# Kernel optimization log

Hardware: AMD Instinct MI355X
Metric: run time of the kernel (lower is better)

Reference implementation:

```python
import jax, jax.numpy as jnp
import numpy as np

N = 50000   # nodes
E = 800000  # edges
G = 256     # graphs in batch
H = 64      # hidden_dim
L = 4       # residual blocks
EPS = 1e-5


def setup_inputs() -> dict:
    key = jax.random.key(0)
    ks = jax.random.split(key, 12)
    s = 0.05
    return dict(
        x=jax.random.normal(ks[0], (N, 3), dtype=jnp.float32),
        edge_index=jax.random.randint(ks[1], (2, E), 0, N, dtype=jnp.int32),
        batch=jnp.sort(jax.random.randint(ks[2], (N,), 0, G, dtype=jnp.int32)),
        proj_W=jax.random.normal(ks[3], (3, H)) * s,
        proj_b=jnp.zeros((H,)),
        conv_W=jax.random.normal(ks[4], (L, 2, H, H)) * s,   # [block, conv1/2, in, out]
        conv_b=jnp.zeros((L, 2, H)),
        bn_g=jnp.ones((L, 2, H)),
        bn_b=jnp.zeros((L, 2, H)),
        lin1_W=jax.random.normal(ks[5], (2 * H, H)) * s,
        lin1_b=jnp.zeros((H,)),
        lin2_W=jax.random.normal(ks[6], (H, H // 2)) * s,
        lin2_b=jnp.zeros((H // 2,)),
        lin3_W=jax.random.normal(ks[7], (H // 2, 2)) * s,
        lin3_b=jnp.zeros((2,)),
        bnf1_g=jnp.ones((H,)), bnf1_b=jnp.zeros((H,)),
        bnf2_g=jnp.ones((H // 2,)), bnf2_b=jnp.zeros((H // 2,)),
    )


def _bn(x, g, b):
    # training-mode BatchNorm1d over the node axis (biased variance)
    m = x.mean(axis=0)
    v = x.var(axis=0)
    return (x - m) * jax.lax.rsqrt(v + EPS) * g + b


def _gcn(h, W, b, src, dst, dis):
    # GCNConv with self-loops and symmetric normalization:
    # out_i = sum_{j->i} d_j^-1/2 d_i^-1/2 (h_j W) + d_i^-1 (h_i W) + b
    hw = h @ W
    msg = hw[src] * (dis[src] * dis[dst])[:, None]          # [E, H] gather
    agg = jax.ops.segment_sum(msg, dst, num_segments=h.shape[0])
    agg = agg + hw * (dis * dis)[:, None]                    # self loops
    return agg + b


def reference(x, edge_index, batch, proj_W, proj_b, conv_W, conv_b, bn_g, bn_b,
              lin1_W, lin1_b, lin2_W, lin2_b, lin3_W, lin3_b,
              bnf1_g, bnf1_b, bnf2_g, bnf2_b):
    src, dst = edge_index[0], edge_index[1]
    n = x.shape[0]
    # degree on A + I (self-loops), computed on destination index
    deg = jax.ops.segment_sum(jnp.ones((src.shape[0],), x.dtype), dst, num_segments=n) + 1.0
    dis = jax.lax.rsqrt(deg)

    h = x @ proj_W + proj_b
    for l in range(L):
        idn = h
        o = _gcn(h, conv_W[l, 0], conv_b[l, 0], src, dst, dis)
        o = jax.nn.relu(_bn(o, bn_g[l, 0], bn_b[l, 0]))
        o = _gcn(o, conv_W[l, 1], conv_b[l, 1], src, dst, dis)
        o = _bn(o, bn_g[l, 1], bn_b[l, 1])
        h = jax.nn.relu(o + idn)

    cnt = jax.ops.segment_sum(jnp.ones((n,), h.dtype), batch, num_segments=G)
    x_mean = jax.ops.segment_sum(h, batch, num_segments=G) / jnp.maximum(cnt, 1.0)[:, None]
    x_max = jax.ops.segment_max(h, batch, num_segments=G)
    x_max = jnp.where(jnp.isfinite(x_max), x_max, 0.0)  # guard empty graphs

    z = jnp.concatenate([x_mean, x_max], axis=1)
    z = jax.nn.relu(_bn(z @ lin1_W + lin1_b, bnf1_g, bnf1_b))
    z = jax.nn.relu(_bn(z @ lin2_W + lin2_b, bnf2_g, bnf2_b))
    return z @ lin3_W + lin3_b
```

## Files before the change

kernel.cpp:

```cpp
#include <hip/hip_runtime.h>
#include <hip/hip_bf16.h>
#include <cstdint>
#include <cstddef>

#define N_NODES 50000
#define N_EDGES 800000
#define G_GRAPHS 256
#define H_DIM 64
#define EPS_BN 1e-5f

__global__ void k_deg(const int* __restrict__ dst, int* __restrict__ cnt) {
    int e = blockIdx.x * 256 + threadIdx.x;
    if (e < N_EDGES) atomicAdd(&cnt[dst[e]], 1);
}

__global__ __launch_bounds__(1024) void k_scan_dis(const int* __restrict__ cnt,
                                                   int* __restrict__ row_ptr,
                                                   float* __restrict__ dis) {
    __shared__ int sh[1024];
    int t = threadIdx.x;
    int base = t * 49;
    int s = 0;
    for (int j = 0; j < 49; j++) {
        int i = base + j;
        if (i < N_NODES) {
            int c = cnt[i];
            dis[i] = rsqrtf((float)c + 1.0f);
            s += c;
        }
    }
    sh[t] = s;
    __syncthreads();
    for (int off = 1; off < 1024; off <<= 1) {
        int v = sh[t];
        int v2 = (t >= off) ? sh[t - off] : 0;
        __syncthreads();
        sh[t] = v + v2;
        __syncthreads();
    }
    int run = sh[t] - s;
    for (int j = 0; j < 49; j++) {
        int i = base + j;
        if (i < N_NODES) { row_ptr[i] = run; run += cnt[i]; }
        else if (i == N_NODES) { row_ptr[i] = run; }
    }
}

__global__ void k_scatter(const int* __restrict__ src, const int* __restrict__ dst,
                          const int* __restrict__ row_ptr, int* __restrict__ cursor,
                          int* __restrict__ csr) {
    int e = blockIdx.x * 256 + threadIdx.x;
    if (e < N_EDGES) {
        int d = dst[e];
        int p = atomicAdd(&cursor[d], 1);
        csr[row_ptr[d] + p] = src[e];
    }
}

__global__ void k_proj(const float* __restrict__ x, const float* __restrict__ W,
                       const float* __restrict__ b, float* __restrict__ h) {
    int tid = blockIdx.x * 256 + threadIdx.x;
    int i = tid >> 6, c = tid & 63;
    if (i < N_NODES) {
        float x0 = x[i * 3], x1 = x[i * 3 + 1], x2 = x[i * 3 + 2];
        h[tid] = x0 * W[c] + x1 * W[64 + c] + x2 * W[128 + c] + b[c];
    }
}

template <int MODE>
__global__ __launch_bounds__(256) void k_gemm(const float* __restrict__ in,
                                              const float* __restrict__ Wg,
                                              const float* __restrict__ dis,
                                              const float* __restrict__ coef,
                                              float* __restrict__ out) {
    __shared__ float Wt[64 * 64];
    __shared__ float hT[64 * 65];
    __shared__ float sA[64], sSh[64];
    int t = threadIdx.x;
    int nb = blockIdx.x * 64;

    if (MODE == 1 && t < 64) { sA[t] = coef[t]; sSh[t] = coef[64 + t]; }
    __syncthreads();

    const float4* W4 = (const float4*)Wg;
    float4* Wt4 = (float4*)Wt;
#pragma unroll
    for (int i = 0; i < 4; i++) Wt4[t + 256 * i] = W4[t + 256 * i];

    int srow = t >> 4, c4 = t & 15;
#pragma unroll
    for (int i = 0; i < 4; i++) {
        int r = srow + 16 * i;
        int node = nb + r;
        float4 v = make_float4(0.f, 0.f, 0.f, 0.f);
        if (node < N_NODES) v = *(const float4*)&in[(size_t)node * 64 + c4 * 4];
        float e0 = v.x, e1 = v.y, e2 = v.z, e3 = v.w;
        if (MODE == 1) {
            int c = c4 * 4;
            e0 = fmaxf(e0 * sA[c] + sSh[c], 0.f);
            e1 = fmaxf(e1 * sA[c + 1] + sSh[c + 1], 0.f);
            e2 = fmaxf(e2 * sA[c + 2] + sSh[c + 2], 0.f);
            e3 = fmaxf(e3 * sA[c + 3] + sSh[c + 3], 0.f);
        }
        float* dr = &hT[r * 65 + c4 * 4];
        dr[0] = e0; dr[1] = e1; dr[2] = e2; dr[3] = e3;
    }
    __syncthreads();

    int c0 = (t & 15) * 4, n0 = (t >> 4) * 4;
    float acc[4][4];
#pragma unroll
    for (int j = 0; j < 4; j++)
#pragma unroll
        for (int i = 0; i < 4; i++) acc[j][i] = 0.f;

#pragma unroll 16
    for (int k = 0; k < 64; k++) {
        float4 wv = *(float4*)&Wt[k * 64 + c0];
        float h0 = hT[(n0 + 0) * 65 + k];
        float h1 = hT[(n0 + 1) * 65 + k];
        float h2 = hT[(n0 + 2) * 65 + k];
        float h3 = hT[(n0 + 3) * 65 + k];
        acc[0][0] += h0 * wv.x; acc[0][1] += h0 * wv.y; acc[0][2] += h0 * wv.z; acc[0][3] += h0 * wv.w;
        acc[1][0] += h1 * wv.x; acc[1][1] += h1 * wv.y; acc[1][2] += h1 * wv.z; acc[1][3] += h1 * wv.w;
        acc[2][0] += h2 * wv.x; acc[2][1] += h2 * wv.y; acc[2][2] += h2 * wv.z; acc[2][3] += h2 * wv.w;
        acc[3][0] += h3 * wv.x; acc[3][1] += h3 * wv.y; acc[3][2] += h3 * wv.z; acc[3][3] += h3 * wv.w;
    }

#pragma unroll
    for (int j = 0; j < 4; j++) {
        int node = nb + n0 + j;
        if (node < N_NODES) {
            float d = dis[node];
            float4 o;
            o.x = acc[j][0] * d; o.y = acc[j][1] * d; o.z = acc[j][2] * d; o.w = acc[j][3] * d;
            *(float4*)&out[(size_t)node * 64 + c0] = o;
        }
    }
}

__global__ __launch_bounds__(256) void k_agg(const float* __restrict__ hwn,
                                             const int* __restrict__ row_ptr,
                                             const int* __restrict__ csr,
                                             const float* __restrict__ dis,
                                             float* __restrict__ o,
                                             float* __restrict__ partial) {
    int t = threadIdx.x;
    int w = t >> 6, lane = t & 63;
    int gw = blockIdx.x * 4 + w;
    float sS = 0.f, sQ = 0.f;
    for (int i = gw; i < N_NODES; i += 4096) {
        float v = hwn[(size_t)i * 64 + lane];
        int beg = row_ptr[i], end = row_ptr[i + 1];
        int e = beg;
        for (; e + 4 <= end; e += 4) {
            int s0 = csr[e], s1 = csr[e + 1], s2 = csr[e + 2], s3 = csr[e + 3];
            float v0 = hwn[(size_t)s0 * 64 + lane];
            float v1 = hwn[(size_t)s1 * 64 + lane];
            float v2 = hwn[(size_t)s2 * 64 + lane];
            float v3 = hwn[(size_t)s3 * 64 + lane];
            v += (v0 + v1) + (v2 + v3);
        }
        for (; e < end; e++) v += hwn[(size_t)csr[e] * 64 + lane];
        v *= dis[i];
        o[(size_t)i * 64 + lane] = v;
        sS += v; sQ += v * v;
    }
    __shared__ float red[4][128];
    red[w][lane] = sS;
    red[w][64 + lane] = sQ;
    __syncthreads();
    if (t < 128) {
        float p = red[0][t] + red[1][t] + red[2][t] + red[3][t];
        partial[blockIdx.x * 128 + t] = p;
    }
}

__global__ __launch_bounds__(512) void k_fin(const float* __restrict__ partial,
                                             const float* __restrict__ g,
                                             const float* __restrict__ b,
                                             float* __restrict__ coef) {
    __shared__ float sh[4][128];
    __shared__ float st[128];
    int t = threadIdx.x;
    int c = t & 127, q = t >> 7;
    float acc = 0.f;
#pragma unroll 4
    for (int r = q; r < 1024; r += 4) acc += partial[r * 128 + c];
    sh[q][c] = acc;
    __syncthreads();
    if (t < 128) st[t] = sh[0][t] + sh[1][t] + sh[2][t] + sh[3][t];
    __syncthreads();
    if (t < 64) {
        float S = st[t], Q = st[t + 64];
        float mean = S * (1.0f / N_NODES);
        float var = Q * (1.0f / N_NODES) - mean * mean;
        float a = g[t] * rsqrtf(var + EPS_BN);
        coef[t] = a;
        coef[64 + t] = b[t] - mean * a;
    }
}

__global__ void k_res(const float* __restrict__ o2, const float* __restrict__ hold,
                      const float* __restrict__ coef, float* __restrict__ hnew) {
    int t4 = blockIdx.x * 256 + threadIdx.x;
    size_t base = (size_t)t4 * 4;
    int c0 = (int)(base & 63);
    float4 o = *(const float4*)&o2[base];
    float4 hi = *(const float4*)&hold[base];
    float4 r;
    r.x = fmaxf(o.x * coef[c0 + 0] + coef[64 + c0 + 0] + hi.x, 0.f);
    r.y = fmaxf(o.y * coef[c0 + 1] + coef[64 + c0 + 1] + hi.y, 0.f);
    r.z = fmaxf(o.z * coef[c0 + 2] + coef[64 + c0 + 2] + hi.z, 0.f);
    r.w = fmaxf(o.w * coef[c0 + 3] + coef[64 + c0 + 3] + hi.w, 0.f);
    *(float4*)&hnew[base] = r;
}

__global__ void k_gbound(const int* __restrict__ batch, int* __restrict__ gstart) {
    int g = threadIdx.x;
    int lo = 0, hi = N_NODES;
    while (lo < hi) {
        int mid = (lo + hi) >> 1;
        if (batch[mid] < g) lo = mid + 1; else hi = mid;
    }
    gstart[g] = lo;
    if (g == 0) gstart[G_GRAPHS] = N_NODES;
}

__global__ __launch_bounds__(256) void k_pool(const float* __restrict__ h,
                                              const int* __restrict__ gstart,
                                              float* __restrict__ pmean,
                                              float* __restrict__ pmax) {
    int g = blockIdx.x;
    int s = gstart[g], e = gstart[g + 1];
    int t = threadIdx.x, w = t >> 6, lane = t & 63;
    float sum = 0.f, mx = 0.f;
    for (int i = s + w; i < e; i += 4) {
        float v = h[(size_t)i * 64 + lane];
        sum += v;
        mx = fmaxf(mx, v);
    }
    __shared__ float rs[4][64], rm[4][64];
    rs[w][lane] = sum;
    rm[w][lane] = mx;
    __syncthreads();
    if (t < 64) {
        float S = rs[0][t] + rs[1][t] + rs[2][t] + rs[3][t];
        float M = fmaxf(fmaxf(rm[0][t], rm[1][t]), fmaxf(rm[2][t], rm[3][t]));
        float cntf = (float)(e - s);
        pmean[g * 64 + t] = S / fmaxf(cntf, 1.0f);
        pmax[g * 64 + t] = M;
    }
}

__global__ __launch_bounds__(512) void k_head(const float* __restrict__ pmean,
                                              const float* __restrict__ pmax,
                                              const float* __restrict__ W1,
                                              const float* __restrict__ W2,
                                              const float* __restrict__ W3,
                                              const float* __restrict__ b3,
                                              const float* __restrict__ g1, const float* __restrict__ bb1,
                                              const float* __restrict__ g2, const float* __restrict__ bb2,
                                              float* __restrict__ ybuf, float* __restrict__ y2buf,
                                              float* __restrict__ outp) {
    int t = threadIdx.x;
    int w = t >> 6, lane = t & 63;
    int rgrp = w & 3, chalf = w >> 2;
    int r = rgrp * 64 + lane;
    __shared__ float pstat[8][32][2];
    __shared__ float aC[64], shC[64];

    float acc[32];
#pragma unroll
    for (int c = 0; c < 32; c++) acc[c] = 0.f;
    int c0 = chalf * 32;
    for (int kc = 0; kc < 4; kc++) {
        float zk[32];
#pragma unroll
        for (int j = 0; j < 32; j++) {
            int k = kc * 32 + j;
            zk[j] = (k < 64) ? pmean[r * 64 + k] : pmax[r * 64 + (k - 64)];
        }
        for (int j = 0; j < 32; j++) {
            float z = zk[j];
            int k = kc * 32 + j;
#pragma unroll
            for (int cq = 0; cq < 8; cq++) {
                float4 wv = *(const float4*)&W1[k * 64 + c0 + cq * 4];
                acc[cq * 4 + 0] += z * wv.x;
                acc[cq * 4 + 1] += z * wv.y;
                acc[cq * 4 + 2] += z * wv.z;
                acc[cq * 4 + 3] += z * wv.w;
            }
        }
    }
    for (int c = 0; c < 32; c++) {
        float v = acc[c], q = acc[c] * acc[c];
        for (int m = 1; m < 64; m <<= 1) { v += __shfl_xor(v, m, 64); q += __shfl_xor(q, m, 64); }
        if (lane == 0) { pstat[w][c][0] = v; pstat[w][c][1] = q; }
    }
    __syncthreads();
    if (t < 64) {
        int ch = t >> 5, cc = t & 31;
        float S = 0.f, Q = 0.f;
        for (int i = 0; i < 4; i++) { S += pstat[ch * 4 + i][cc][0]; Q += pstat[ch * 4 + i][cc][1]; }
        float mean = S * (1.f / 256.f), var = Q * (1.f / 256.f) - mean * mean;
        float a = g1[t] * rsqrtf(var + EPS_BN);
        aC[t] = a;
        shC[t] = bb1[t] - mean * a;
    }
    __syncthreads();
    for (int c = 0; c < 32; c++) {
        float y = fmaxf(acc[c] * aC[c0 + c] + shC[c0 + c], 0.f);
        ybuf[r * 64 + c0 + c] = y;
    }
    __syncthreads();

    float acc2[16];
#pragma unroll
    for (int c = 0; c < 16; c++) acc2[c] = 0.f;
    int c0b = chalf * 16;
    for (int kc = 0; kc < 2; kc++) {
        float yk[32];
#pragma unroll
        for (int j = 0; j < 32; j++) yk[j] = ybuf[r * 64 + kc * 32 + j];
        for (int j = 0; j < 32; j++) {
            float y = yk[j];
            int k = kc * 32 + j;
#pragma unroll
            for (int cq = 0; cq < 4; cq++) {
                float4 wv = *(const float4*)&W2[k * 32 + c0b + cq * 4];
                acc2[cq * 4 + 0] += y * wv.x;
                acc2[cq * 4 + 1] += y * wv.y;
                acc2[cq * 4 + 2] += y * wv.z;
                acc2[cq * 4 + 3] += y * wv.w;
            }
        }
    }
    for (int c = 0; c < 16; c++) {
        float v = acc2[c], q = acc2[c] * acc2[c];
        for (int m = 1; m < 64; m <<= 1) { v += __shfl_xor(v, m, 64); q += __shfl_xor(q, m, 64); }
        if (lane == 0) { pstat[w][c][0] = v; pstat[w][c][1] = q; }
    }
    __syncthreads();
    if (t < 32) {
        int ch = t >> 4, cc = t & 15;
        float S = 0.f, Q = 0.f;
        for (int i = 0; i < 4; i++) { S += pstat[ch * 4 + i][cc][0]; Q += pstat[ch * 4 + i][cc][1]; }
        float mean = S * (1.f / 256.f), var = Q * (1.f / 256.f) - mean * mean;
        float a = g2[t] * rsqrtf(var + EPS_BN);
        aC[t] = a;
        shC[t] = bb2[t] - mean * a;
    }
    __syncthreads();
    for (int c = 0; c < 16; c++) {
        float y = fmaxf(acc2[c] * aC[c0b + c] + shC[c0b + c], 0.f);
        y2buf[r * 32 + c0b + c] = y;
    }
    __syncthreads();

    if (chalf == 0) {
        float o0 = b3[0], o1 = b3[1];
        for (int j = 0; j < 32; j++) {
            float y = y2buf[r * 32 + j];
            o0 += y * W3[j * 2];
            o1 += y * W3[j * 2 + 1];
        }
        outp[r * 2] = o0;
        outp[r * 2 + 1] = o1;
    }
}

extern "C" void kernel_launch(void* const* d_in, const int* in_sizes, int n_in,
                              void* d_out, int out_size, void* d_ws, size_t ws_size,
                              hipStream_t stream) {
    (void)in_sizes; (void)n_in; (void)out_size; (void)ws_size;
    const float* x      = (const float*)d_in[0];
    const int*   ei     = (const int*)d_in[1];
    const int*   batch  = (const int*)d_in[2];
    const float* proj_W = (const float*)d_in[3];
    const float* proj_b = (const float*)d_in[4];
    const float* conv_W = (const float*)d_in[5];
    const float* bn_g   = (const float*)d_in[7];
    const float* bn_b   = (const float*)d_in[8];
    const float* lin1_W = (const float*)d_in[9];
    const float* lin2_W = (const float*)d_in[11];
    const float* lin3_W = (const float*)d_in[13];
    const float* lin3_b = (const float*)d_in[14];
    const float* bnf1_g = (const float*)d_in[15];
    const float* bnf1_b = (const float*)d_in[16];
    const float* bnf2_g = (const float*)d_in[17];
    const float* bnf2_b = (const float*)d_in[18];
    const int* srcp = ei;
    const int* dstp = ei + N_EDGES;

    char* ws = (char*)d_ws;
    auto alloc = [&](size_t bytes) {
        char* p = ws;
        ws += (bytes + 255) / 256 * 256;
        return p;
    };
    int*   cnt     = (int*)alloc((size_t)N_NODES * 4);
    float* dis     = (float*)alloc((size_t)N_NODES * 4);
    int*   row_ptr = (int*)alloc((size_t)(N_NODES + 1) * 4);
    int*   cursor  = (int*)alloc((size_t)N_NODES * 4);
    int*   csr     = (int*)alloc((size_t)N_EDGES * 4);
    float* BA      = (float*)alloc((size_t)N_NODES * 64 * 4);
    float* BB      = (float*)alloc((size_t)N_NODES * 64 * 4);
    float* BC      = (float*)alloc((size_t)N_NODES * 64 * 4);
    float* partial = (float*)alloc((size_t)1024 * 128 * 4);
    float* coef    = (float*)alloc(128 * 4);
    float* pmean   = (float*)alloc((size_t)G_GRAPHS * 64 * 4);
    float* pmax    = (float*)alloc((size_t)G_GRAPHS * 64 * 4);
    int*   gstart  = (int*)alloc((size_t)(G_GRAPHS + 1) * 4);
    float* ybuf    = (float*)alloc((size_t)G_GRAPHS * 64 * 4);
    float* y2buf   = (float*)alloc((size_t)G_GRAPHS * 32 * 4);

    hipMemsetAsync(cnt, 0, (size_t)N_NODES * 4, stream);
    hipMemsetAsync(cursor, 0, (size_t)N_NODES * 4, stream);

    k_deg<<<3125, 256, 0, stream>>>(dstp, cnt);
    k_scan_dis<<<1, 1024, 0, stream>>>(cnt, row_ptr, dis);
    k_scatter<<<3125, 256, 0, stream>>>(srcp, dstp, row_ptr, cursor, csr);
    k_proj<<<12500, 256, 0, stream>>>(x, proj_W, proj_b, BA);

    float* A = BA; float* B = BB; float* C = BC;
    for (int l = 0; l < 4; l++) {
        const float* W0 = conv_W + (size_t)(l * 2 + 0) * 4096;
        const float* W1c = conv_W + (size_t)(l * 2 + 1) * 4096;
        k_gemm<0><<<782, 256, 0, stream>>>(A, W0, dis, nullptr, B);
        k_agg<<<1024, 256, 0, stream>>>(B, row_ptr, csr, dis, C, partial);
        k_fin<<<1, 512, 0, stream>>>(partial, bn_g + (l * 2) * 64, bn_b + (l * 2) * 64, coef);
        k_gemm<1><<<782, 256, 0, stream>>>(C, W1c, dis, coef, B);
        k_agg<<<1024, 256, 0, stream>>>(B, row_ptr, csr, dis, C, partial);
        k_fin<<<1, 512, 0, stream>>>(partial, bn_g + (l * 2 + 1) * 64, bn_b + (l * 2 + 1) * 64, coef);
        k_res<<<3125, 256, 0, stream>>>(C, A, coef, B);
        float* t0 = A; A = B; B = C; C = t0;
    }

    k_gbound<<<1, 256, 0, stream>>>(batch, gstart);
    k_pool<<<256, 256, 0, stream>>>(A, gstart, pmean, pmax);
    k_head<<<1, 512, 0, stream>>>(pmean, pmax, lin1_W, lin2_W, lin3_W, lin3_b,
                                  bnf1_g, bnf1_b, bnf2_g, bnf2_b, ybuf, y2buf, (float*)d_out);
}
```

Baseline: 1.213 ms.

## Replace BN partial reduction with atomics, split head, merge memsets, fold gbound

The BN statistics in k_agg are now accumulated with global float atomics into a zeroed stats buffer, so the finalize kernel becomes a tiny 64-thread kernel instead of reducing 1024 partials. k_agg grid doubles to 2048 blocks. The single-block MLP head is split into three kernels, two of them spread over 32 blocks with atomic BN stats. Graph-boundary search moves into k_pool, and the two memsets merge into one covering cnt, cursor and stats. Float atomics make the BN sums order-nondeterministic.

```diff
diff --git a/kernel.cpp b/kernel.cpp
--- a/kernel.cpp
+++ b/kernel.cpp
@@ -144,12 +144,12 @@
                                              const int* __restrict__ csr,
                                              const float* __restrict__ dis,
                                              float* __restrict__ o,
-                                             float* __restrict__ partial) {
+                                             float* __restrict__ astat) {
     int t = threadIdx.x;
     int w = t >> 6, lane = t & 63;
     int gw = blockIdx.x * 4 + w;
     float sS = 0.f, sQ = 0.f;
-    for (int i = gw; i < N_NODES; i += 4096) {
+    for (int i = gw; i < N_NODES; i += 8192) {
         float v = hwn[(size_t)i * 64 + lane];
         int beg = row_ptr[i], end = row_ptr[i + 1];
         int e = beg;
@@ -172,33 +172,21 @@
     __syncthreads();
     if (t < 128) {
         float p = red[0][t] + red[1][t] + red[2][t] + red[3][t];
-        partial[blockIdx.x * 128 + t] = p;
-    }
-}
-
-__global__ __launch_bounds__(512) void k_fin(const float* __restrict__ partial,
-                                             const float* __restrict__ g,
-                                             const float* __restrict__ b,
-                                             float* __restrict__ coef) {
-    __shared__ float sh[4][128];
-    __shared__ float st[128];
-    int t = threadIdx.x;
-    int c = t & 127, q = t >> 7;
-    float acc = 0.f;
-#pragma unroll 4
-    for (int r = q; r < 1024; r += 4) acc += partial[r * 128 + c];
-    sh[q][c] = acc;
-    __syncthreads();
-    if (t < 128) st[t] = sh[0][t] + sh[1][t] + sh[2][t] + sh[3][t];
-    __syncthreads();
-    if (t < 64) {
-        float S = st[t], Q = st[t + 64];
-        float mean = S * (1.0f / N_NODES);
-        float var = Q * (1.0f / N_NODES) - mean * mean;
-        float a = g[t] * rsqrtf(var + EPS_BN);
-        coef[t] = a;
-        coef[64 + t] = b[t] - mean * a;
-    }
+        atomicAdd(&astat[t], p);
+    }
+}
+
+__global__ void k_fin(const float* __restrict__ astat,
+                      const float* __restrict__ g,
+                      const float* __restrict__ b,
+                      float* __restrict__ coef) {
+    int t = threadIdx.x;
+    float S = astat[t], Q = astat[64 + t];
+    float mean = S * (1.0f / N_NODES);
+    float var = Q * (1.0f / N_NODES) - mean * mean;
+    float a = g[t] * rsqrtf(var + EPS_BN);
+    coef[t] = a;
+    coef[64 + t] = b[t] - mean * a;
 }
 
 __global__ void k_res(const float* __restrict__ o2, const float* __restrict__ hold,
@@ -216,23 +204,17 @@
     *(float4*)&hnew[base] = r;
 }
 
-__global__ void k_gbound(const int* __restrict__ batch, int* __restrict__ gstart) {
-    int g = threadIdx.x;
-    int lo = 0, hi = N_NODES;
-    while (lo < hi) {
-        int mid = (lo + hi) >> 1;
-        if (batch[mid] < g) lo = mid + 1; else hi = mid;
-    }
-    gstart[g] = lo;
-    if (g == 0) gstart[G_GRAPHS] = N_NODES;
-}
-
 __global__ __launch_bounds__(256) void k_pool(const float* __restrict__ h,
-                                              const int* __restrict__ gstart,
+                                              const int* __restrict__ batch,
                                               float* __restrict__ pmean,
                                               float* __restrict__ pmax) {
     int g = blockIdx.x;
-    int s = gstart[g], e = gstart[g + 1];
+    int lo = 0, hi = N_NODES;
+    while (lo < hi) { int mid = (lo + hi) >> 1; if (batch[mid] < g) lo = mid + 1; else hi = mid; }
+    int s = lo;
+    hi = N_NODES;
+    while (lo < hi) { int mid = (lo + hi) >> 1; if (batch[mid] < g + 1) lo = mid + 1; else hi = mid; }
+    int e = lo;
     int t = threadIdx.x, w = t >> 6, lane = t & 63;
     float sum = 0.f, mx = 0.f;
     for (int i = s + w; i < e; i += 4) {
@@ -253,122 +235,103 @@
     }
 }
 
-__global__ __launch_bounds__(512) void k_head(const float* __restrict__ pmean,
-                                              const float* __restrict__ pmax,
-                                              const float* __restrict__ W1,
-                                              const float* __restrict__ W2,
-                                              const float* __restrict__ W3,
-                                              const float* __restrict__ b3,
-                                              const float* __restrict__ g1, const float* __restrict__ bb1,
-                                              const float* __restrict__ g2, const float* __restrict__ bb2,
-                                              float* __restrict__ ybuf, float* __restrict__ y2buf,
-                                              float* __restrict__ outp) {
-    int t = threadIdx.x;
-    int w = t >> 6, lane = t & 63;
-    int rgrp = w & 3, chalf = w >> 2;
-    int r = rgrp * 64 + lane;
-    __shared__ float pstat[8][32][2];
-    __shared__ float aC[64], shC[64];
-
-    float acc[32];
-#pragma unroll
-    for (int c = 0; c < 32; c++) acc[c] = 0.f;
-    int c0 = chalf * 32;
-    for (int kc = 0; kc < 4; kc++) {
-        float zk[32];
-#pragma unroll
-        for (int j = 0; j < 32; j++) {
-            int k = kc * 32 + j;
-            zk[j] = (k < 64) ? pmean[r * 64 + k] : pmax[r * 64 + (k - 64)];
-        }
-        for (int j = 0; j < 32; j++) {
-            float z = zk[j];
-            int k = kc * 32 + j;
-#pragma unroll
-            for (int cq = 0; cq < 8; cq++) {
-                float4 wv = *(const float4*)&W1[k * 64 + c0 + cq * 4];
-                acc[cq * 4 + 0] += z * wv.x;
-                acc[cq * 4 + 1] += z * wv.y;
-                acc[cq * 4 + 2] += z * wv.z;
-                acc[cq * 4 + 3] += z * wv.w;
-            }
-        }
-    }
-    for (int c = 0; c < 32; c++) {
-        float v = acc[c], q = acc[c] * acc[c];
-        for (int m = 1; m < 64; m <<= 1) { v += __shfl_xor(v, m, 64); q += __shfl_xor(q, m, 64); }
-        if (lane == 0) { pstat[w][c][0] = v; pstat[w][c][1] = q; }
-    }
-    __syncthreads();
+__global__ __launch_bounds__(256) void k_head1(const float* __restrict__ pmean,
+                                               const float* __restrict__ pmax,
+                                               const float* __restrict__ W1,
+                                               float* __restrict__ z1,
+                                               float* __restrict__ hstat1) {
+    __shared__ float bs[128];
+    int t = threadIdx.x;
+    int row = blockIdx.x * 8 + (t >> 5);
+    int col2 = (t & 31) * 2;
+    if (t < 128) bs[t] = 0.f;
+    __syncthreads();
+    float acc0 = 0.f, acc1 = 0.f;
+    const float* zr = &pmean[row * 64];
+    for (int k = 0; k < 64; k++) {
+        float zv = zr[k];
+        float2 wv = *(const float2*)&W1[k * 64 + col2];
+        acc0 += zv * wv.x; acc1 += zv * wv.y;
+    }
+    const float* zr2 = &pmax[row * 64];
+    for (int k = 0; k < 64; k++) {
+        float zv = zr2[k];
+        float2 wv = *(const float2*)&W1[(64 + k) * 64 + col2];
+        acc0 += zv * wv.x; acc1 += zv * wv.y;
+    }
+    *(float2*)&z1[row * 64 + col2] = make_float2(acc0, acc1);
+    atomicAdd(&bs[col2], acc0);
+    atomicAdd(&bs[col2 + 1], acc1);
+    atomicAdd(&bs[64 + col2], acc0 * acc0);
+    atomicAdd(&bs[64 + col2 + 1], acc1 * acc1);
+    __syncthreads();
+    if (t < 128) atomicAdd(&hstat1[t], bs[t]);
+}
+
+__global__ __launch_bounds__(256) void k_head2(const float* __restrict__ z1,
+                                               const float* __restrict__ W2,
+                                               const float* __restrict__ hstat1,
+                                               const float* __restrict__ g1,
+                                               const float* __restrict__ bb1,
+                                               float* __restrict__ z2,
+                                               float* __restrict__ hstat2) {
+    __shared__ float aC[64], shC[64], ys[8][64], bs2[64];
+    int t = threadIdx.x;
     if (t < 64) {
-        int ch = t >> 5, cc = t & 31;
-        float S = 0.f, Q = 0.f;
-        for (int i = 0; i < 4; i++) { S += pstat[ch * 4 + i][cc][0]; Q += pstat[ch * 4 + i][cc][1]; }
-        float mean = S * (1.f / 256.f), var = Q * (1.f / 256.f) - mean * mean;
+        float S = hstat1[t], Q = hstat1[64 + t];
+        float mean = S * (1.f / 256.f);
+        float var = Q * (1.f / 256.f) - mean * mean;
         float a = g1[t] * rsqrtf(var + EPS_BN);
-        aC[t] = a;
-        shC[t] = bb1[t] - mean * a;
-    }
-    __syncthreads();
-    for (int c = 0; c < 32; c++) {
-        float y = fmaxf(acc[c] * aC[c0 + c] + shC[c0 + c], 0.f);
-        ybuf[r * 64 + c0 + c] = y;
-    }
-    __syncthreads();
-
-    float acc2[16];
-#pragma unroll
-    for (int c = 0; c < 16; c++) acc2[c] = 0.f;
-    int c0b = chalf * 16;
-    for (int kc = 0; kc < 2; kc++) {
-        float yk[32];
-#pragma unroll
-        for (int j = 0; j < 32; j++) yk[j] = ybuf[r * 64 + kc * 32 + j];
-        for (int j = 0; j < 32; j++) {
-            float y = yk[j];
-            int k = kc * 32 + j;
-#pragma unroll
-            for (int cq = 0; cq < 4; cq++) {
-                float4 wv = *(const float4*)&W2[k * 32 + c0b + cq * 4];
-                acc2[cq * 4 + 0] += y * wv.x;
-                acc2[cq * 4 + 1] += y * wv.y;
-                acc2[cq * 4 + 2] += y * wv.z;
-                acc2[cq * 4 + 3] += y * wv.w;
-            }
-        }
-    }
-    for (int c = 0; c < 16; c++) {
-        float v = acc2[c], q = acc2[c] * acc2[c];
-        for (int m = 1; m < 64; m <<= 1) { v += __shfl_xor(v, m, 64); q += __shfl_xor(q, m, 64); }
-        if (lane == 0) { pstat[w][c][0] = v; pstat[w][c][1] = q; }
-    }
-    __syncthreads();
+        aC[t] = a; shC[t] = bb1[t] - mean * a;
+        bs2[t] = 0.f;
+    }
+    __syncthreads();
+    for (int i = t; i < 512; i += 256) {
+        int rl = i >> 6, k = i & 63;
+        float v = z1[(blockIdx.x * 8 + rl) * 64 + k];
+        ys[rl][k] = fmaxf(v * aC[k] + shC[k], 0.f);
+    }
+    __syncthreads();
+    int rl = t >> 5, col = t & 31;
+    float acc = 0.f;
+    for (int k = 0; k < 64; k++) acc += ys[rl][k] * W2[k * 32 + col];
+    z2[(blockIdx.x * 8 + rl) * 32 + col] = acc;
+    atomicAdd(&bs2[col], acc);
+    atomicAdd(&bs2[32 + col], acc * acc);
+    __syncthreads();
+    if (t < 64) atomicAdd(&hstat2[t], bs2[t]);
+}
+
+__global__ __launch_bounds__(256) void k_head3(const float* __restrict__ z2,
+                                               const float* __restrict__ W3,
+                                               const float* __restrict__ b3,
+                                               const float* __restrict__ hstat2,
+                                               const float* __restrict__ g2,
+                                               const float* __restrict__ bb2,
+                                               float* __restrict__ outp) {
+    __shared__ float aC[32], shC[32];
+    __shared__ float y2s[256 * 33];
+    int t = threadIdx.x;
     if (t < 32) {
-        int ch = t >> 4, cc = t & 15;
-        float S = 0.f, Q = 0.f;
-        for (int i = 0; i < 4; i++) { S += pstat[ch * 4 + i][cc][0]; Q += pstat[ch * 4 + i][cc][1]; }
-        float mean = S * (1.f / 256.f), var = Q * (1.f / 256.f) - mean * mean;
+        float S = hstat2[t], Q = hstat2[32 + t];
+        float mean = S * (1.f / 256.f);
+        float var = Q * (1.f / 256.f) - mean * mean;
         float a = g2[t] * rsqrtf(var + EPS_BN);
-        aC[t] = a;
-        shC[t] = bb2[t] - mean * a;
-    }
-    __syncthreads();
-    for (int c = 0; c < 16; c++) {
-        float y = fmaxf(acc2[c] * aC[c0b + c] + shC[c0b + c], 0.f);
-        y2buf[r * 32 + c0b + c] = y;
-    }
-    __syncthreads();
-
-    if (chalf == 0) {
-        float o0 = b3[0], o1 = b3[1];
-        for (int j = 0; j < 32; j++) {
-            float y = y2buf[r * 32 + j];
-            o0 += y * W3[j * 2];
-            o1 += y * W3[j * 2 + 1];
-        }
-        outp[r * 2] = o0;
-        outp[r * 2 + 1] = o1;
-    }
+        aC[t] = a; shC[t] = bb2[t] - mean * a;
+    }
+    __syncthreads();
+    for (int i = t; i < 8192; i += 256) {
+        int r = i >> 5, k = i & 31;
+        y2s[r * 33 + k] = fmaxf(z2[i] * aC[k] + shC[k], 0.f);
+    }
+    __syncthreads();
+    float o0 = b3[0], o1 = b3[1];
+    const float* yr = &y2s[t * 33];
+    for (int k = 0; k < 32; k++) {
+        float y = yr[k];
+        o0 += y * W3[k * 2]; o1 += y * W3[k * 2 + 1];
+    }
+    outp[t * 2] = o0; outp[t * 2 + 1] = o1;
 }
 
 extern "C" void kernel_launch(void* const* d_in, const int* in_sizes, int n_in,
@@ -401,23 +364,26 @@
         return p;
     };
     int*   cnt     = (int*)alloc((size_t)N_NODES * 4);
+    int*   cursor  = (int*)alloc((size_t)N_NODES * 4);
+    float* stats   = (float*)alloc((size_t)1216 * 4);
+    size_t zero_bytes = (size_t)ws - (size_t)d_ws;
+
     float* dis     = (float*)alloc((size_t)N_NODES * 4);
     int*   row_ptr = (int*)alloc((size_t)(N_NODES + 1) * 4);
-    int*   cursor  = (int*)alloc((size_t)N_NODES * 4);
     int*   csr     = (int*)alloc((size_t)N_EDGES * 4);
     float* BA      = (float*)alloc((size_t)N_NODES * 64 * 4);
     float* BB      = (float*)alloc((size_t)N_NODES * 64 * 4);
     float* BC      = (float*)alloc((size_t)N_NODES * 64 * 4);
-    float* partial = (float*)alloc((size_t)1024 * 128 * 4);
     float* coef    = (float*)alloc(128 * 4);
     float* pmean   = (float*)alloc((size_t)G_GRAPHS * 64 * 4);
     float* pmax    = (float*)alloc((size_t)G_GRAPHS * 64 * 4);
-    int*   gstart  = (int*)alloc((size_t)(G_GRAPHS + 1) * 4);
-    float* ybuf    = (float*)alloc((size_t)G_GRAPHS * 64 * 4);
-    float* y2buf   = (float*)alloc((size_t)G_GRAPHS * 32 * 4);
-
-    hipMemsetAsync(cnt, 0, (size_t)N_NODES * 4, stream);
-    hipMemsetAsync(cursor, 0, (size_t)N_NODES * 4, stream);
+    float* z1buf   = (float*)alloc((size_t)G_GRAPHS * 64 * 4);
+    float* z2buf   = (float*)alloc((size_t)G_GRAPHS * 32 * 4);
+
+    float* hstat1 = stats + 1024;
+    float* hstat2 = stats + 1024 + 128;
+
+    hipMemsetAsync(d_ws, 0, zero_bytes, stream);
 
     k_deg<<<3125, 256, 0, stream>>>(dstp, cnt);
     k_scan_dis<<<1, 1024, 0, stream>>>(cnt, row_ptr, dis);
@@ -428,18 +394,20 @@
     for (int l = 0; l < 4; l++) {
         const float* W0 = conv_W + (size_t)(l * 2 + 0) * 4096;
         const float* W1c = conv_W + (size_t)(l * 2 + 1) * 4096;
+        float* st0 = stats + (size_t)(l * 2 + 0) * 128;
+        float* st1 = stats + (size_t)(l * 2 + 1) * 128;
         k_gemm<0><<<782, 256, 0, stream>>>(A, W0, dis, nullptr, B);
-        k_agg<<<1024, 256, 0, stream>>>(B, row_ptr, csr, dis, C, partial);
-        k_fin<<<1, 512, 0, stream>>>(partial, bn_g + (l * 2) * 64, bn_b + (l * 2) * 64, coef);
+        k_agg<<<2048, 256, 0, stream>>>(B, row_ptr, csr, dis, C, st0);
+        k_fin<<<1, 64, 0, stream>>>(st0, bn_g + (l * 2) * 64, bn_b + (l * 2) * 64, coef);
         k_gemm<1><<<782, 256, 0, stream>>>(C, W1c, dis, coef, B);
-        k_agg<<<1024, 256, 0, stream>>>(B, row_ptr, csr, dis, C, partial);
-        k_fin<<<1, 512, 0, stream>>>(partial, bn_g + (l * 2 + 1) * 64, bn_b + (l * 2 + 1) * 64, coef);
+        k_agg<<<2048, 256, 0, stream>>>(B, row_ptr, csr, dis, C, st1);
+        k_fin<<<1, 64, 0, stream>>>(st1, bn_g + (l * 2 + 1) * 64, bn_b + (l * 2 + 1) * 64, coef);
         k_res<<<3125, 256, 0, stream>>>(C, A, coef, B);
         float* t0 = A; A = B; B = C; C = t0;
     }
 
-    k_gbound<<<1, 256, 0, stream>>>(batch, gstart);
-    k_pool<<<256, 256, 0, stream>>>(A, gstart, pmean, pmax);
-    k_head<<<1, 512, 0, stream>>>(pmean, pmax, lin1_W, lin2_W, lin3_W, lin3_b,
-                                  bnf1_g, bnf1_b, bnf2_g, bnf2_b, ybuf, y2buf, (float*)d_out);
-}
+    k_pool<<<256, 256, 0, stream>>>(A, batch, pmean, pmax);
+    k_head1<<<32, 256, 0, stream>>>(pmean, pmax, lin1_W, z1buf, hstat1);
+    k_head2<<<32, 256, 0, stream>>>(z1buf, lin2_W, hstat1, bnf1_g, bnf1_b, z2buf, hstat2);
+    k_head3<<<1, 256, 0, stream>>>(z2buf, lin3_W, lin3_b, hstat2, bnf2_g, bnf2_b, (float*)d_out);
+}
```

Result: faster. 1.144 ms (-5.7%).
